# Performance work log

Measured on AMD Instinct MI355X. Metric: run time of the kernel, lower is better.

The kernel has to match this reference:

```python
import jax, jax.numpy as jnp
import numpy as np

LN_EPS = 1e-5


def _layer_norm(x, scale, bias):
    mu = jnp.mean(x, axis=-1, keepdims=True)
    var = jnp.mean(jnp.square(x - mu), axis=-1, keepdims=True)
    return (x - mu) * jax.lax.rsqrt(var + LN_EPS) * scale + bias


def setup_inputs() -> dict:
    key = jax.random.key(0)
    B, N, C_Z, C_H = 1, 512, 128, 128
    ks = jax.random.split(key, 8)
    s = 1.0 / np.sqrt(C_Z)
    inp = {
        "z": jax.random.normal(ks[0], (B, N, N, C_Z), dtype=jnp.float32),
        "mask": jnp.ones((B, N, N), dtype=jnp.float32),
        # gated / plain projections from c_z -> c_hidden
        "w_a_p": jax.random.normal(ks[1], (C_Z, C_H), dtype=jnp.float32) * s,
        "b_a_p": jnp.zeros((C_H,), dtype=jnp.float32),
        "w_a_g": jnp.zeros((C_Z, C_H), dtype=jnp.float32),  # gating init: zeros, bias ones
        "b_a_g": jnp.ones((C_H,), dtype=jnp.float32),
        "w_b_p": jax.random.normal(ks[2], (C_Z, C_H), dtype=jnp.float32) * s,
        "b_b_p": jnp.zeros((C_H,), dtype=jnp.float32),
        "w_b_g": jnp.zeros((C_Z, C_H), dtype=jnp.float32),
        "b_b_g": jnp.ones((C_H,), dtype=jnp.float32),
        # output gate c_z -> c_z (gating init)
        "w_g": jnp.zeros((C_Z, C_Z), dtype=jnp.float32),
        "b_g": jnp.ones((C_Z,), dtype=jnp.float32),
        # final projection c_hidden -> c_z ('final' init: zeros; use small randn for a nontrivial test)
        "w_z": jax.random.normal(ks[3], (C_H, C_Z), dtype=jnp.float32) * (1.0 / np.sqrt(C_H)),
        "b_z": jnp.zeros((C_Z,), dtype=jnp.float32),
        "ln_in_scale": jnp.ones((C_Z,), dtype=jnp.float32),
        "ln_in_bias": jnp.zeros((C_Z,), dtype=jnp.float32),
        "ln_out_scale": jnp.ones((C_H,), dtype=jnp.float32),
        "ln_out_bias": jnp.zeros((C_H,), dtype=jnp.float32),
    }
    return inp


def reference(z, mask, w_a_p, b_a_p, w_a_g, b_a_g, w_b_p, b_b_p, w_b_g, b_b_g,
              w_g, b_g, w_z, b_z, ln_in_scale, ln_in_bias, ln_out_scale, ln_out_bias):
    # tmu_type == 'outgoing'
    z = _layer_norm(z, ln_in_scale, ln_in_bias)          # [B,N,N,Cz]
    m = mask[..., None]                                   # [B,N,N,1]
    a = jax.nn.sigmoid(z @ w_a_g + b_a_g) * m * (z @ w_a_p + b_a_p)  # [B,N,N,Ch]
    b = jax.nn.sigmoid(z @ w_b_g + b_b_g) * m * (z @ w_b_p + b_b_p)  # [B,N,N,Ch]
    # outgoing: p[b,i,j,c] = sum_k a[b,i,k,c] * b[b,j,k,c]
    x = jnp.einsum("bikc,bjkc->bijc", a, b)              # [B,N,N,Ch]
    x = _layer_norm(x, ln_out_scale, ln_out_bias)
    x = x @ w_z + b_z                                    # [B,N,N,Cz]
    g = jax.nn.sigmoid(z @ w_g + b_g)                    # [B,N,N,Cz]
    return x * g
```

## Files before the change

### kernel.cpp

```cpp
#include <hip/hip_runtime.h>

typedef __attribute__((ext_vector_type(8))) short short8;
typedef __attribute__((ext_vector_type(4))) short short4v;
typedef __attribute__((ext_vector_type(4))) float float4v;

#define NDIM 512
#define NN (NDIM*NDIM)
#define CD 128

__device__ __forceinline__ unsigned short f2b(float f) {
  union { float f; unsigned u; } v; v.f = f;
  unsigned r = v.u + 0x7FFFu + ((v.u >> 16) & 1u);
  return (unsigned short)(r >> 16);
}
__device__ __forceinline__ float b2f(unsigned short h) {
  union { unsigned u; float f; } v; v.u = ((unsigned)h) << 16; return v.f;
}
__device__ __forceinline__ float sigmoidf_(float x) {
  return __fdividef(1.f, 1.f + __expf(-x));
}
__device__ __forceinline__ unsigned pk2(float a, float b) {
  unsigned r;
  asm("v_cvt_pk_bf16_f32 %0, %1, %2" : "=v"(r) : "v"(a), "v"(b));
  return r;
}
__device__ __forceinline__ float4v mfma16(short8 a, short8 b, float4v c) {
  return __builtin_amdgcn_mfma_f32_16x16x32_bf16(a, b, c, 0, 0, 0);
}
__device__ __forceinline__ void gl_lds16(const short* g, short* l) {
  __builtin_amdgcn_global_load_lds(
      (const __attribute__((address_space(1))) unsigned int*)g,
      (__attribute__((address_space(3))) unsigned int*)l, 16, 0, 0);
}

__device__ __forceinline__ short8 fragr(const short* buf, int row, int j) {
  return *(const short8*)(buf + row * 128 + ((j ^ (row & 15)) << 3));
}
__device__ __forceinline__ void stg_w(short* buf, int row, int ku, unsigned v) {
  *(unsigned*)&buf[row * 128 + ((((ku >> 2) ^ (row & 15)) << 3) + ((ku & 3) << 1))] = v;
}
__device__ __forceinline__ void stg_w2(short* buf, int row, int ku, unsigned v0, unsigned v1) {
  unsigned long long v = (unsigned long long)v0 | ((unsigned long long)v1 << 32);
  *(unsigned long long*)&buf[row * 128 + ((((ku >> 2) ^ (row & 15)) << 3) + ((ku & 3) << 1))] = v;
}

__global__ __launch_bounds__(256) void kPrepW(
    const float* __restrict__ w0, const float* __restrict__ w1,
    const float* __restrict__ w2, const float* __restrict__ w3,
    const float* __restrict__ w4, short* __restrict__ wt)
{
  const int wi = blockIdx.y;
  const float* W = wi==0 ? w0 : wi==1 ? w1 : wi==2 ? w2 : wi==3 ? w3 : w4;
  const int e = blockIdx.x * 256 + threadIdx.x;
  const int k = e >> 7, n = e & 127;
  wt[wi * 16384 + n * 128 + k] = (short)f2b(W[k * CD + n]);
}

__global__ __launch_bounds__(1024, 4) void kProj(
    const float* __restrict__ z, const float* __restrict__ mask,
    const short* __restrict__ wT,
    const float* __restrict__ b_a_p, const float* __restrict__ b_a_g,
    const float* __restrict__ b_b_p, const float* __restrict__ b_b_g,
    const float* __restrict__ b_g,
    const float* __restrict__ ln_s, const float* __restrict__ ln_b,
    short* __restrict__ a_t, short* __restrict__ b_t, short* __restrict__ g_out)
{
  __shared__ short zln[128 * 128];
  __shared__ short sS[128 * 128];
  __shared__ short wA[128 * 128];
  __shared__ short wB[128 * 128];
  const int t = threadIdx.x;
  const int r0 = blockIdx.x * 128;
  const int w = t >> 6, l = t & 63, lr = l & 15, lg = l >> 4;
  const int wr = (w >> 1) * 16;
  const int hc = (w & 1) * 64;

#define STAGE2(BUF, SLOT) do { _Pragma("unroll") for (int i_=0;i_<2;++i_) {  \
    int U_ = i_*1024 + t; int row_ = U_ >> 4, u_ = U_ & 15;                  \
    gl_lds16(wT + (SLOT)*16384 + row_*128 + ((u_^(row_&15))<<3), (BUF)+U_*8); } } while(0)

  STAGE2(wA, 1);
  STAGE2(wB, 0);

  {
    const int row = t >> 3, q = t & 7;
    const float* zp = z + (size_t)(r0 + row) * CD + q * 16;
    float x[16];
#pragma unroll
    for (int i = 0; i < 4; ++i) {
      float4v v = *(const float4v*)(zp + i * 4);
#pragma unroll
      for (int e = 0; e < 4; ++e) x[i*4+e] = v[e];
    }
    float s = 0.f;
#pragma unroll
    for (int i = 0; i < 16; ++i) s += x[i];
    s += __shfl_xor(s, 1, 64);
    s += __shfl_xor(s, 2, 64);
    s += __shfl_xor(s, 4, 64);
    const float mu = s * (1.f/128.f);
    float vs = 0.f;
#pragma unroll
    for (int i = 0; i < 16; ++i) { float d = x[i]-mu; vs += d*d; }
    vs += __shfl_xor(vs, 1, 64);
    vs += __shfl_xor(vs, 2, 64);
    vs += __shfl_xor(vs, 4, 64);
    const float rstd = rsqrtf(vs * (1.f/128.f) + 1e-5f);
#pragma unroll
    for (int i = 0; i < 16; i += 4) {
      int c = q*16 + i;
      float y0 = (x[i]  -mu)*rstd*ln_s[c]   + ln_b[c];
      float y1 = (x[i+1]-mu)*rstd*ln_s[c+1] + ln_b[c+1];
      float y2 = (x[i+2]-mu)*rstd*ln_s[c+2] + ln_b[c+2];
      float y3 = (x[i+3]-mu)*rstd*ln_s[c+3] + ln_b[c+3];
      int addr = row*128 + (((c>>3) ^ (row & 15)) << 3) + (c & 7);
      unsigned long long pv = (unsigned long long)pk2(y0, y1)
                            | ((unsigned long long)pk2(y2, y3) << 32);
      *(unsigned long long*)(&zln[addr]) = pv;
    }
  }

  float bga[4], bpa[4], bgb[4], bpb[4];
#pragma unroll
  for (int cf = 0; cf < 4; ++cf) {
    int ci = hc + cf*16 + lr;
    bga[cf] = b_a_g[ci]; bpa[cf] = b_a_p[ci];
    bgb[cf] = b_b_g[ci]; bpb[cf] = b_b_p[ci];
  }
  float mrow[4];
#pragma unroll
  for (int jj = 0; jj < 4; ++jj) mrow[jj] = mask[r0 + wr + lg*4 + jj];

  __syncthreads();

  short8 af[4];
#pragma unroll
  for (int ks = 0; ks < 4; ++ks)
    af[ks] = fragr(zln, wr + lr, ks*4 + lg);

  float4v accG[4], accB[4];
  float sg[4][4];

#define ZERO4(A) do { _Pragma("unroll") for (int c_=0;c_<4;++c_) A[c_] = (float4v){0.f,0.f,0.f,0.f}; } while(0)

#define WP(ACC, BUF) do { ZERO4(ACC);                                      \
  _Pragma("unroll") for (int ks_=0; ks_<4; ++ks_)                          \
    _Pragma("unroll") for (int cf_=0; cf_<4; ++cf_) {                      \
      short8 wf_ = fragr(BUF, hc + cf_*16 + lr, ks_*4 + lg);               \
      ACC[cf_] = mfma16(af[ks_], wf_, ACC[cf_]);                           \
    } } while(0)

#define SIG4(BG) do { _Pragma("unroll") for (int cf_=0;cf_<4;++cf_)        \
    _Pragma("unroll") for (int j_=0;j_<4;++j_)                             \
      sg[cf_][j_] = sigmoidf_(accG[cf_][j_] + BG[cf_]) * mrow[j_]; } while(0)

#define PKAB(BP) do { _Pragma("unroll") for (int cf_=0;cf_<4;++cf_) {      \
    float v0_ = sg[cf_][0]*(accB[cf_][0]+BP[cf_]);                         \
    float v1_ = sg[cf_][1]*(accB[cf_][1]+BP[cf_]);                         \
    float v2_ = sg[cf_][2]*(accB[cf_][2]+BP[cf_]);                         \
    float v3_ = sg[cf_][3]*(accB[cf_][3]+BP[cf_]);                         \
    int ch_ = hc + cf_*16 + lr, ku_ = (wr >> 1) + lg*2;                    \
    stg_w2(sS, ch_, ku_, pk2(v0_, v1_), pk2(v2_, v3_)); } } while(0)

#define STORE64A(DST) do { int ch_ = t >> 3;                               \
  _Pragma("unroll") for (int i_=0;i_<2;++i_) {                             \
    int cL_ = (t & 7)*2 + i_;                                              \
    *(short8*)(DST + (size_t)ch_*NN + r0 + cL_*8) = fragr(sS, ch_, cL_);   \
  } } while(0)

  WP(accG, wA);
  WP(accB, wB);
  SIG4(bga);
  PKAB(bpa);
  __syncthreads();

  STAGE2(wA, 3);
  STAGE2(wB, 2);
  STAGE2(zln, 4);
  STORE64A(a_t);
  __syncthreads();

  WP(accG, wA);
  WP(accB, wB);
  float4v accG2[4];
  ZERO4(accG2);
#pragma unroll
  for (int ks = 0; ks < 4; ++ks)
#pragma unroll
    for (int cf = 0; cf < 4; ++cf) {
      short8 wf = fragr(zln, hc + cf*16 + lr, ks*4 + lg);
      accG2[cf] = mfma16(wf, af[ks], accG2[cf]);
    }
  SIG4(bgb);
  PKAB(bpb);
  __syncthreads();

  STORE64A(b_t);
#pragma unroll
  for (int cf = 0; cf < 4; ++cf) {
    float4v bgv = *(const float4v*)(b_g + hc + cf*16 + lg*4);
    float v0 = sigmoidf_(accG2[cf][0] + bgv[0]);
    float v1 = sigmoidf_(accG2[cf][1] + bgv[1]);
    float v2 = sigmoidf_(accG2[cf][2] + bgv[2]);
    float v3 = sigmoidf_(accG2[cf][3] + bgv[3]);
    int row = wr + lr, ku = (hc >> 1) + cf*8 + lg*2;
    stg_w2(zln, row, ku, pk2(v0, v1), pk2(v2, v3));
  }
  __syncthreads();

  {
    int row = t >> 3;
#pragma unroll
    for (int i = 0; i < 2; ++i) {
      int cL = (t & 7)*2 + i;
      *(short8*)(g_out + (size_t)(r0 + row)*CD + cL*8) = fragr(zln, row, cL);
    }
  }
}

__global__ __launch_bounds__(256, 2) void kEinsum(const short* __restrict__ a_t,
                                                  const short* __restrict__ b_t,
                                                  short* __restrict__ x_t)
{
  __shared__ short As[2][128 * 64];
  __shared__ short Bs[2][128 * 64];
  const int t = threadIdx.x;
  const int d = blockIdx.x;
  const int c = (d & 7) * 16 + (d >> 7);
  const int tile = (d >> 3) & 15;
  const int i0 = (tile >> 2) * 128;
  const int j0 = (tile & 3) * 128;
  const size_t abase = (size_t)c * NN;
  const int w = t >> 6, l = t & 63, lr = l & 15, lg = l >> 4;
  const int wr = w >> 1, wc = w & 1;

  const short* gA[4]; const short* gB[4]; int ldsU[4];
#pragma unroll
  for (int q = 0; q < 4; ++q) {
    int U = q * 256 + t;
    int row = U >> 3, u = U & 7;
    int swz = ((u ^ (row & 7)) << 3);
    gA[q] = a_t + abase + (size_t)(i0 + row) * NDIM + swz;
    gB[q] = b_t + abase + (size_t)(j0 + row) * NDIM + swz;
    ldsU[q] = U * 8;
  }

#define STAGE_E(buf, k0) do { _Pragma("unroll") for (int q_=0;q_<4;++q_) { \
    gl_lds16(gA[q_] + (k0), &As[buf][ldsU[q_]]);                           \
    gl_lds16(gB[q_] + (k0), &Bs[buf][ldsU[q_]]); } } while(0)

  float4v acc[4][4];
#pragma unroll
  for (int m = 0; m < 4; ++m)
#pragma unroll
    for (int n = 0; n < 4; ++n) acc[m][n] = (float4v){0.f,0.f,0.f,0.f};

  STAGE_E(0, 0);
  STAGE_E(1, 64);
#pragma unroll
  for (int it = 0; it < 8; ++it) {
    if (it < 7) asm volatile("s_waitcnt vmcnt(8)" ::: "memory");
    else        asm volatile("s_waitcnt vmcnt(0)" ::: "memory");
    __builtin_amdgcn_sched_barrier(0);
    __builtin_amdgcn_s_barrier();
    const short* Ab = &As[it & 1][0];
    const short* Bb = &Bs[it & 1][0];
    short8 afr[4][2], bfr[4][2];
#pragma unroll
    for (int m = 0; m < 4; ++m)
#pragma unroll
      for (int ks = 0; ks < 2; ++ks) {
        int row = wr*64 + m*16 + lr, j = ks*4 + lg;
        afr[m][ks] = *(const short8*)(Ab + row*64 + ((j ^ (row & 7)) << 3));
      }
#pragma unroll
    for (int n = 0; n < 4; ++n)
#pragma unroll
      for (int ks = 0; ks < 2; ++ks) {
        int row = wc*64 + n*16 + lr, j = ks*4 + lg;
        bfr[n][ks] = *(const short8*)(Bb + row*64 + ((j ^ (row & 7)) << 3));
      }
    __builtin_amdgcn_s_setprio(1);
#pragma unroll
    for (int ks = 0; ks < 2; ++ks)
#pragma unroll
      for (int m = 0; m < 4; ++m)
#pragma unroll
        for (int n = 0; n < 4; ++n)
          acc[m][n] = mfma16(bfr[n][ks], afr[m][ks], acc[m][n]);
    __builtin_amdgcn_s_setprio(0);
    __builtin_amdgcn_s_barrier();
    __builtin_amdgcn_sched_barrier(0);
    if (it < 6) STAGE_E(it & 1, (it + 2) * 64);
  }
  short* Xs = &As[0][0];
#pragma unroll
  for (int m = 0; m < 4; ++m)
#pragma unroll
    for (int n = 0; n < 4; ++n) {
      int il = wr*64 + m*16 + lr;
      int ku = wc*32 + n*8 + lg*2;
      stg_w2(Xs, il, ku, pk2(acc[m][n][0], acc[m][n][1]),
                         pk2(acc[m][n][2], acc[m][n][3]));
    }
  __syncthreads();
#pragma unroll
  for (int i = 0; i < 8; ++i) {
    int il = t >> 1, cL = (t & 1)*8 + i;
    *(short8*)(x_t + abase + (size_t)(i0 + il)*NDIM + j0 + cL*8) = fragr(Xs, il, cL);
  }
}

__global__ __launch_bounds__(1024, 4) void kOut(
    const short* __restrict__ x_t, const short* __restrict__ g_in,
    const float* __restrict__ w_z, const float* __restrict__ b_z,
    const float* __restrict__ ln_s, const float* __restrict__ ln_b,
    float* __restrict__ out)
{
  __shared__ short xs[128 * 128];
  __shared__ short xln[128 * 128];
  __shared__ short sW[128 * 128];
  const int t = threadIdx.x;
  const int r0 = blockIdx.x * 128;
  const int w = t >> 6, l = t & 63, lr = l & 15, lg = l >> 4;
  const int rowb = (w >> 1) * 16;
  const int hc = (w & 1) * 64;

  short8 gv[2];
#pragma unroll
  for (int v = 0; v < 2; ++v) {
    int V = v*1024 + t; int row = V >> 4, u = V & 15;
    gv[v] = *(const short8*)(g_in + (size_t)(r0 + row) * CD + u * 8);
  }
#pragma unroll
  for (int v = 0; v < 2; ++v) {
    int U = v*1024 + t; int cc = U >> 4, u = U & 15;
    gl_lds16(x_t + (size_t)cc * NN + r0 + ((u ^ ((cc >> 3) & 15)) << 3), xs + U*8);
  }
#pragma unroll
  for (int i = 0; i < 2; ++i) {
    int flat = i*1024 + t;
    int kp = flat >> 5, k = kp * 2, n4 = (flat & 31) * 4;
    float4v va = *(const float4v*)(w_z + (size_t)k * CD + n4);
    float4v vb = *(const float4v*)(w_z + (size_t)(k + 1) * CD + n4);
#pragma unroll
    for (int j = 0; j < 4; ++j) {
      int row = n4 + j;
      int addr = row * 128 + (((k >> 3) ^ (row & 15)) << 3) + (k & 7);
      *(unsigned*)(&sW[addr]) = pk2(va[j], vb[j]);
    }
  }
  __syncthreads();
  {
    const int r = t >> 3, q = t & 7;
    float x[16];
#pragma unroll
    for (int i = 0; i < 16; ++i) {
      int c = q*16 + i;
      x[i] = b2f((unsigned short)xs[c*128 + (((r >> 3) ^ ((c >> 3) & 15)) << 3) + (r & 7)]);
    }
    float s = 0.f;
#pragma unroll
    for (int i = 0; i < 16; ++i) s += x[i];
    s += __shfl_xor(s, 1, 64);
    s += __shfl_xor(s, 2, 64);
    s += __shfl_xor(s, 4, 64);
    const float mu = s * (1.f/128.f);
    float vs = 0.f;
#pragma unroll
    for (int i = 0; i < 16; ++i) { float d = x[i]-mu; vs += d*d; }
    vs += __shfl_xor(vs, 1, 64);
    vs += __shfl_xor(vs, 2, 64);
    vs += __shfl_xor(vs, 4, 64);
    const float rstd = rsqrtf(vs * (1.f/128.f) + 1e-5f);
#pragma unroll
    for (int i = 0; i < 16; i += 4) {
      int c = q*16 + i;
      float y0 = (x[i]  -mu)*rstd*ln_s[c]   + ln_b[c];
      float y1 = (x[i+1]-mu)*rstd*ln_s[c+1] + ln_b[c+1];
      float y2 = (x[i+2]-mu)*rstd*ln_s[c+2] + ln_b[c+2];
      float y3 = (x[i+3]-mu)*rstd*ln_s[c+3] + ln_b[c+3];
      int addr = r*128 + (((c>>3) ^ (r & 15)) << 3) + (c & 7);
      unsigned long long pv = (unsigned long long)pk2(y0, y1)
                            | ((unsigned long long)pk2(y2, y3) << 32);
      *(unsigned long long*)(&xln[addr]) = pv;
    }
  }
  __syncthreads();
  short* sG = xs;
#pragma unroll
  for (int v = 0; v < 2; ++v) {
    int V = v*1024 + t; int row = V >> 4, u = V & 15;
    *(short8*)(sG + row*128 + ((u ^ (row & 15)) << 3)) = gv[v];
  }
  short8 af[4];
#pragma unroll
  for (int ks = 0; ks < 4; ++ks)
    af[ks] = fragr(xln, rowb + lr, ks*4 + lg);
  float4v acc[4];
#pragma unroll
  for (int cf = 0; cf < 4; ++cf) acc[cf] = (float4v){0.f,0.f,0.f,0.f};
#pragma unroll
  for (int ks = 0; ks < 4; ++ks)
#pragma unroll
    for (int cf = 0; cf < 4; ++cf) {
      short8 wf = fragr(sW, hc + cf*16 + lr, ks*4 + lg);
      acc[cf] = mfma16(af[ks], wf, acc[cf]);
    }
  float bz[4];
#pragma unroll
  for (int cf = 0; cf < 4; ++cf) bz[cf] = b_z[hc + cf*16 + lr];
  __syncthreads();
#pragma unroll
  for (int cf = 0; cf < 4; ++cf) {
    int ch = hc + cf*16 + lr;
#pragma unroll
    for (int jj = 0; jj < 4; ++jj) {
      int row = rowb + lg*4 + jj;
      float gvv = b2f((unsigned short)sG[row*128 + (((ch>>3) ^ (row & 15)) << 3) + (ch & 7)]);
      out[(size_t)(r0 + row) * CD + ch] = (acc[cf][jj] + bz[cf]) * gvv;
    }
  }
}

extern "C" void kernel_launch(void* const* d_in, const int* in_sizes, int n_in,
                              void* d_out, int out_size, void* d_ws, size_t ws_size,
                              hipStream_t stream) {
  (void)in_sizes; (void)n_in; (void)out_size; (void)ws_size;
  const float* z     = (const float*)d_in[0];
  const float* mask  = (const float*)d_in[1];
  const float* w_a_p = (const float*)d_in[2];
  const float* b_a_p = (const float*)d_in[3];
  const float* w_a_g = (const float*)d_in[4];
  const float* b_a_g = (const float*)d_in[5];
  const float* w_b_p = (const float*)d_in[6];
  const float* b_b_p = (const float*)d_in[7];
  const float* w_b_g = (const float*)d_in[8];
  const float* b_b_g = (const float*)d_in[9];
  const float* w_g   = (const float*)d_in[10];
  const float* b_g   = (const float*)d_in[11];
  const float* w_z   = (const float*)d_in[12];
  const float* b_z   = (const float*)d_in[13];
  const float* ln_i_s = (const float*)d_in[14];
  const float* ln_i_b = (const float*)d_in[15];
  const float* ln_o_s = (const float*)d_in[16];
  const float* ln_o_b = (const float*)d_in[17];

  short* a_t = (short*)d_ws;
  short* b_t = a_t + (size_t)CD*NN;
  short* g_s = b_t + (size_t)CD*NN;
  short* x_t = g_s + (size_t)CD*NN;
  short* wT  = x_t;

  hipLaunchKernelGGL(kPrepW, dim3(64, 5), dim3(256), 0, stream,
                     w_a_p, w_a_g, w_b_p, w_b_g, w_g, wT);
  hipLaunchKernelGGL(kProj, dim3(NN/128), dim3(1024), 0, stream,
                     z, mask, wT, b_a_p, b_a_g, b_b_p, b_b_g, b_g,
                     ln_i_s, ln_i_b, a_t, b_t, g_s);
  hipLaunchKernelGGL(kEinsum, dim3(2048), dim3(256), 0, stream, a_t, b_t, x_t);
  hipLaunchKernelGGL(kOut, dim3(NN/128), dim3(1024), 0, stream,
                     x_t, g_s, w_z, b_z, ln_o_s, ln_o_b, (float*)d_out);
}
```

Before: 308.9 us.

## Split kProj blocks by channel half to cut LDS and raise occupancy

Each kProj block now handles 128 rows by 64 output channels with 512 threads, instead of all 128 channels with 1024 threads. This shrinks the weight and staging LDS buffers so more blocks can fit per CU. A block-index swizzle keeps the two channel halves of the same rows on the same XCD, so the duplicated z read and layer norm can hit L2. The cost is that every z row is loaded and normalized twice.

```diff
diff --git a/kernel.cpp b/kernel.cpp
--- a/kernel.cpp
+++ b/kernel.cpp
@@ -56,7 +56,7 @@
   wt[wi * 16384 + n * 128 + k] = (short)f2b(W[k * CD + n]);
 }
 
-__global__ __launch_bounds__(1024, 4) void kProj(
+__global__ __launch_bounds__(512, 4) void kProj(
     const float* __restrict__ z, const float* __restrict__ mask,
     const short* __restrict__ wT,
     const float* __restrict__ b_a_p, const float* __restrict__ b_a_g,
@@ -66,49 +66,50 @@
     short* __restrict__ a_t, short* __restrict__ b_t, short* __restrict__ g_out)
 {
   __shared__ short zln[128 * 128];
-  __shared__ short sS[128 * 128];
-  __shared__ short wA[128 * 128];
-  __shared__ short wB[128 * 128];
+  __shared__ short sS[64 * 128];
+  __shared__ short wA[64 * 128];
+  __shared__ short wB[64 * 128];
   const int t = threadIdx.x;
-  const int r0 = blockIdx.x * 128;
+  const int bid = blockIdx.x;
+  const int sw = (bid & 7) * 512 + (bid >> 3);
+  const int ch_half = sw & 1;
+  const int r0 = (sw >> 1) * 128;
+  const int choff = ch_half * 64;
   const int w = t >> 6, l = t & 63, lr = l & 15, lg = l >> 4;
-  const int wr = (w >> 1) * 16;
-  const int hc = (w & 1) * 64;
-
-#define STAGE2(BUF, SLOT) do { _Pragma("unroll") for (int i_=0;i_<2;++i_) {  \
-    int U_ = i_*1024 + t; int row_ = U_ >> 4, u_ = U_ & 15;                  \
-    gl_lds16(wT + (SLOT)*16384 + row_*128 + ((u_^(row_&15))<<3), (BUF)+U_*8); } } while(0)
-
-  STAGE2(wA, 1);
-  STAGE2(wB, 0);
+  const int wr = w * 16;
+
+#define STAGE2H(BUF, SLOT) do { _Pragma("unroll") for (int i_=0;i_<2;++i_) {        \
+    int U_ = i_*512 + t; int row_ = U_ >> 4, u_ = U_ & 15;                          \
+    gl_lds16(wT + (SLOT)*16384 + (choff + row_)*128 + ((u_^(row_&15))<<3), (BUF)+U_*8); } } while(0)
+
+  STAGE2H(wA, 1);
+  STAGE2H(wB, 0);
 
   {
-    const int row = t >> 3, q = t & 7;
-    const float* zp = z + (size_t)(r0 + row) * CD + q * 16;
-    float x[16];
-#pragma unroll
-    for (int i = 0; i < 4; ++i) {
+    const int row = t >> 2, q = t & 3;
+    const float* zp = z + (size_t)(r0 + row) * CD + q * 32;
+    float x[32];
+#pragma unroll
+    for (int i = 0; i < 8; ++i) {
       float4v v = *(const float4v*)(zp + i * 4);
 #pragma unroll
       for (int e = 0; e < 4; ++e) x[i*4+e] = v[e];
     }
     float s = 0.f;
 #pragma unroll
-    for (int i = 0; i < 16; ++i) s += x[i];
+    for (int i = 0; i < 32; ++i) s += x[i];
     s += __shfl_xor(s, 1, 64);
     s += __shfl_xor(s, 2, 64);
-    s += __shfl_xor(s, 4, 64);
     const float mu = s * (1.f/128.f);
     float vs = 0.f;
 #pragma unroll
-    for (int i = 0; i < 16; ++i) { float d = x[i]-mu; vs += d*d; }
+    for (int i = 0; i < 32; ++i) { float d = x[i]-mu; vs += d*d; }
     vs += __shfl_xor(vs, 1, 64);
     vs += __shfl_xor(vs, 2, 64);
-    vs += __shfl_xor(vs, 4, 64);
     const float rstd = rsqrtf(vs * (1.f/128.f) + 1e-5f);
 #pragma unroll
-    for (int i = 0; i < 16; i += 4) {
-      int c = q*16 + i;
+    for (int i = 0; i < 32; i += 4) {
+      int c = q*32 + i;
       float y0 = (x[i]  -mu)*rstd*ln_s[c]   + ln_b[c];
       float y1 = (x[i+1]-mu)*rstd*ln_s[c+1] + ln_b[c+1];
       float y2 = (x[i+2]-mu)*rstd*ln_s[c+2] + ln_b[c+2];
@@ -123,7 +124,7 @@
   float bga[4], bpa[4], bgb[4], bpb[4];
 #pragma unroll
   for (int cf = 0; cf < 4; ++cf) {
-    int ci = hc + cf*16 + lr;
+    int ci = choff + cf*16 + lr;
     bga[cf] = b_a_g[ci]; bpa[cf] = b_a_p[ci];
     bgb[cf] = b_b_g[ci]; bpb[cf] = b_b_p[ci];
   }
@@ -146,7 +147,7 @@
 #define WP(ACC, BUF) do { ZERO4(ACC);                                      \
   _Pragma("unroll") for (int ks_=0; ks_<4; ++ks_)                          \
     _Pragma("unroll") for (int cf_=0; cf_<4; ++cf_) {                      \
-      short8 wf_ = fragr(BUF, hc + cf_*16 + lr, ks_*4 + lg);               \
+      short8 wf_ = fragr(BUF, cf_*16 + lr, ks_*4 + lg);                    \
       ACC[cf_] = mfma16(af[ks_], wf_, ACC[cf_]);                           \
     } } while(0)
 
@@ -159,13 +160,13 @@
     float v1_ = sg[cf_][1]*(accB[cf_][1]+BP[cf_]);                         \
     float v2_ = sg[cf_][2]*(accB[cf_][2]+BP[cf_]);                         \
     float v3_ = sg[cf_][3]*(accB[cf_][3]+BP[cf_]);                         \
-    int ch_ = hc + cf_*16 + lr, ku_ = (wr >> 1) + lg*2;                    \
+    int ch_ = cf_*16 + lr, ku_ = (wr >> 1) + lg*2;                         \
     stg_w2(sS, ch_, ku_, pk2(v0_, v1_), pk2(v2_, v3_)); } } while(0)
 
 #define STORE64A(DST) do { int ch_ = t >> 3;                               \
   _Pragma("unroll") for (int i_=0;i_<2;++i_) {                             \
     int cL_ = (t & 7)*2 + i_;                                              \
-    *(short8*)(DST + (size_t)ch_*NN + r0 + cL_*8) = fragr(sS, ch_, cL_);   \
+    *(short8*)(DST + (size_t)(choff + ch_)*NN + r0 + cL_*8) = fragr(sS, ch_, cL_); \
   } } while(0)
 
   WP(accG, wA);
@@ -174,9 +175,9 @@
   PKAB(bpa);
   __syncthreads();
 
-  STAGE2(wA, 3);
-  STAGE2(wB, 2);
-  STAGE2(zln, 4);
+  STAGE2H(wA, 3);
+  STAGE2H(wB, 2);
+  STAGE2H(zln, 4);
   STORE64A(a_t);
   __syncthreads();
 
@@ -188,7 +189,7 @@
   for (int ks = 0; ks < 4; ++ks)
 #pragma unroll
     for (int cf = 0; cf < 4; ++cf) {
-      short8 wf = fragr(zln, hc + cf*16 + lr, ks*4 + lg);
+      short8 wf = fragr(zln, cf*16 + lr, ks*4 + lg);
       accG2[cf] = mfma16(wf, af[ks], accG2[cf]);
     }
   SIG4(bgb);
@@ -198,22 +199,22 @@
   STORE64A(b_t);
 #pragma unroll
   for (int cf = 0; cf < 4; ++cf) {
-    float4v bgv = *(const float4v*)(b_g + hc + cf*16 + lg*4);
+    float4v bgv = *(const float4v*)(b_g + choff + cf*16 + lg*4);
     float v0 = sigmoidf_(accG2[cf][0] + bgv[0]);
     float v1 = sigmoidf_(accG2[cf][1] + bgv[1]);
     float v2 = sigmoidf_(accG2[cf][2] + bgv[2]);
     float v3 = sigmoidf_(accG2[cf][3] + bgv[3]);
-    int row = wr + lr, ku = (hc >> 1) + cf*8 + lg*2;
+    int row = wr + lr, ku = cf*8 + lg*2;
     stg_w2(zln, row, ku, pk2(v0, v1), pk2(v2, v3));
   }
   __syncthreads();
 
   {
-    int row = t >> 3;
+    int row = t >> 2;
 #pragma unroll
     for (int i = 0; i < 2; ++i) {
-      int cL = (t & 7)*2 + i;
-      *(short8*)(g_out + (size_t)(r0 + row)*CD + cL*8) = fragr(zln, row, cL);
+      int cL = (t & 3)*2 + i;
+      *(short8*)(g_out + (size_t)(r0 + row)*CD + choff + cL*8) = fragr(zln, row, cL);
     }
   }
 }
@@ -454,7 +455,7 @@
 
   hipLaunchKernelGGL(kPrepW, dim3(64, 5), dim3(256), 0, stream,
                      w_a_p, w_a_g, w_b_p, w_b_g, w_g, wT);
-  hipLaunchKernelGGL(kProj, dim3(NN/128), dim3(1024), 0, stream,
+  hipLaunchKernelGGL(kProj, dim3(4096), dim3(512), 0, stream,
                      z, mask, wT, b_a_p, b_a_g, b_b_p, b_b_g, b_g,
                      ln_i_s, ln_i_b, a_t, b_t, g_s);
   hipLaunchKernelGGL(kEinsum, dim3(2048), dim3(256), 0, stream, a_t, b_t, x_t);
```

Result: no change. 313.0 us (+1.3%).
